# Performance work log

Hardware: AMD Instinct MI355X
Metric: run time of the kernel (lower is better)

The kernel has to match this reference:

```python
import jax, jax.numpy as jnp
import numpy as np

B, A, E, H, W = 128, 256, 256, 64, 64


def setup_inputs() -> dict:
    key = jax.random.key(0)
    k1, k2, k3 = jax.random.split(key, 3)
    action = jax.random.normal(k1, (B, A), dtype=jnp.float32)
    # Conv2d(A, E, kernel_size=1) weight is [E, A, 1, 1]; store as [E, A]
    conv_w = jax.random.normal(k2, (E, A), dtype=jnp.float32) * (1.0 / np.sqrt(A))
    conv_b = jax.random.normal(k3, (E,), dtype=jnp.float32) * 0.01
    return {"action": action, "conv_w": conv_w, "conv_b": conv_b}


def reference(action, conv_w, conv_b):
    # Tiling the action across HxW then applying a 1x1 conv is mathematically a
    # per-sample linear layer whose result is broadcast over spatial positions.
    # y[b, e] = relu(sum_a action[b, a] * conv_w[e, a] + conv_b[e])
    y = jax.nn.relu(jnp.einsum('ba,ea->be', action, conv_w) + conv_b)  # [B, E]
    # Broadcast to the full [B, E, H, W] output, identical to conv over tiles.
    return jnp.broadcast_to(y[:, :, None, None], (y.shape[0], y.shape[1], H, W))
```

## Files before the change

kernel.cpp:

```cpp
#include <hip/hip_runtime.h>

#define B_DIM 128
#define A_DIM 256
#define E_DIM 256
#define HW    4096

typedef float f32x4 __attribute__((ext_vector_type(4)));

__global__ void __launch_bounds__(256) compute_y_kernel(
    const float* __restrict__ action,
    const float* __restrict__ conv_w,
    const float* __restrict__ conv_b,
    float* __restrict__ y)
{
    const int b = blockIdx.x;
    const int e = threadIdx.x;

    __shared__ float act[A_DIM];
    act[e] = action[b * A_DIM + e];
    __syncthreads();

    const float4* w4 = reinterpret_cast<const float4*>(conv_w + e * A_DIM);
    const float4* a4 = reinterpret_cast<const float4*>(act);

    float sum = conv_b[e];
    #pragma unroll
    for (int i = 0; i < A_DIM / 4; ++i) {
        float4 w = w4[i];
        float4 a = a4[i];
        sum = fmaf(a.x, w.x, sum);
        sum = fmaf(a.y, w.y, sum);
        sum = fmaf(a.z, w.z, sum);
        sum = fmaf(a.w, w.w, sum);
    }
    y[b * E_DIM + e] = fmaxf(sum, 0.0f);
}

__global__ void __launch_bounds__(256) broadcast_y_kernel(
    const float* __restrict__ y,
    f32x4* __restrict__ out)
{
    const int t = threadIdx.x;
    f32x4* dst = out + (size_t)blockIdx.x * 16384 + t;
    const int ybase = blockIdx.x * 16;

    #pragma unroll
    for (int k = 0; k < 16; ++k) {
        const float v = y[ybase + k];
        const f32x4 v4 = {v, v, v, v};
        #pragma unroll
        for (int j = 0; j < 4; ++j) {
            dst[k * 1024 + j * 256] = v4;
        }
    }
}

extern "C" void kernel_launch(void* const* d_in, const int* in_sizes, int n_in,
                              void* d_out, int out_size, void* d_ws, size_t ws_size,
                              hipStream_t stream) {
    const float* action = (const float*)d_in[0];
    const float* conv_w = (const float*)d_in[1];
    const float* conv_b = (const float*)d_in[2];
    float* out = (float*)d_out;
    float* y   = (float*)d_ws;

    compute_y_kernel<<<B_DIM, 256, 0, stream>>>(action, conv_w, conv_b, y);

    broadcast_y_kernel<<<2048, 256, 0, stream>>>(
        y, reinterpret_cast<f32x4*>(out));
}
```

Baseline: 531.3 us.

## Fuse linear+ReLU computation into broadcast kernel with per-block shuffle reductions

Merges the GEMV kernel and the broadcast kernel into one launch. Each block computes its own 16 output scalars, with 16 lanes per scalar doing a partial dot product followed by a shuffle reduction. The scalars are staged in shared memory, and the block then writes their broadcast over 4096 spatial positions. This removes a kernel launch, the workspace round trip and the serialization between the two kernels. In exchange, every block reloads its weight and action rows, and the stores now wait on a dot product and a barrier.

```diff
diff --git a/kernel.cpp b/kernel.cpp
--- a/kernel.cpp
+++ b/kernel.cpp
@@ -4,53 +4,57 @@
 #define A_DIM 256
 #define E_DIM 256
 #define HW    4096
+#define CHUNKS_PER_BLOCK 16
+#define NBLOCKS (B_DIM * E_DIM / CHUNKS_PER_BLOCK)
 
 typedef float f32x4 __attribute__((ext_vector_type(4)));
 
-__global__ void __launch_bounds__(256) compute_y_kernel(
+__global__ void __launch_bounds__(256) fused_embed_kernel(
     const float* __restrict__ action,
     const float* __restrict__ conv_w,
     const float* __restrict__ conv_b,
-    float* __restrict__ y)
-{
-    const int b = blockIdx.x;
-    const int e = threadIdx.x;
-
-    __shared__ float act[A_DIM];
-    act[e] = action[b * A_DIM + e];
-    __syncthreads();
-
-    const float4* w4 = reinterpret_cast<const float4*>(conv_w + e * A_DIM);
-    const float4* a4 = reinterpret_cast<const float4*>(act);
-
-    float sum = conv_b[e];
-    #pragma unroll
-    for (int i = 0; i < A_DIM / 4; ++i) {
-        float4 w = w4[i];
-        float4 a = a4[i];
-        sum = fmaf(a.x, w.x, sum);
-        sum = fmaf(a.y, w.y, sum);
-        sum = fmaf(a.z, w.z, sum);
-        sum = fmaf(a.w, w.w, sum);
-    }
-    y[b * E_DIM + e] = fmaxf(sum, 0.0f);
-}
-
-__global__ void __launch_bounds__(256) broadcast_y_kernel(
-    const float* __restrict__ y,
     f32x4* __restrict__ out)
 {
     const int t = threadIdx.x;
-    f32x4* dst = out + (size_t)blockIdx.x * 16384 + t;
-    const int ybase = blockIdx.x * 16;
+    const int ybase = blockIdx.x * CHUNKS_PER_BLOCK;
+    const int g = t >> 4;
+    const int l = t & 15;
+    const int be = ybase + g;
+    const int b  = be >> 8;
+    const int e  = be & 255;
 
+    const float4* a4 = reinterpret_cast<const float4*>(action + b * A_DIM + l * 16);
+    const float4* w4 = reinterpret_cast<const float4*>(conv_w + e * A_DIM + l * 16);
+    float s = 0.0f;
     #pragma unroll
-    for (int k = 0; k < 16; ++k) {
-        const float v = y[ybase + k];
-        const f32x4 v4 = {v, v, v, v};
+    for (int i = 0; i < 4; ++i) {
+        float4 a = a4[i];
+        float4 w = w4[i];
+        s = fmaf(a.x, w.x, s);
+        s = fmaf(a.y, w.y, s);
+        s = fmaf(a.z, w.z, s);
+        s = fmaf(a.w, w.w, s);
+    }
+    s += __shfl_xor(s, 8, 16);
+    s += __shfl_xor(s, 4, 16);
+    s += __shfl_xor(s, 2, 16);
+    s += __shfl_xor(s, 1, 16);
+
+    __shared__ float ysm[CHUNKS_PER_BLOCK];
+    if (l == 0) ysm[g] = fmaxf(s + conv_b[e], 0.0f);
+    __syncthreads();
+
+    float yv[CHUNKS_PER_BLOCK];
+    #pragma unroll
+    for (int k = 0; k < CHUNKS_PER_BLOCK; ++k) yv[k] = ysm[k];
+
+    f32x4* dst = out + (size_t)blockIdx.x * (CHUNKS_PER_BLOCK * HW / 4) + t;
+    #pragma unroll
+    for (int k = 0; k < CHUNKS_PER_BLOCK; ++k) {
+        const f32x4 v4 = {yv[k], yv[k], yv[k], yv[k]};
         #pragma unroll
         for (int j = 0; j < 4; ++j) {
-            dst[k * 1024 + j * 256] = v4;
+            dst[k * (HW / 4) + j * 256] = v4;
         }
     }
 }
@@ -61,11 +65,7 @@
     const float* action = (const float*)d_in[0];
     const float* conv_w = (const float*)d_in[1];
     const float* conv_b = (const float*)d_in[2];
-    float* out = (float*)d_out;
-    float* y   = (float*)d_ws;
 
-    compute_y_kernel<<<B_DIM, 256, 0, stream>>>(action, conv_w, conv_b, y);
-
-    broadcast_y_kernel<<<2048, 256, 0, stream>>>(
-        y, reinterpret_cast<f32x4*>(out));
+    fused_embed_kernel<<<NBLOCKS, 256, 0, stream>>>(
+        action, conv_w, conv_b, reinterpret_cast<f32x4*>(d_out));
 }
```

Result: no change. 521.1 us (-1.9%).
